# Kernel tuning notes

Measured on AMD Instinct MI355X. Metric: run time of the kernel, lower is better.

The kernel has to match this reference:

```python
import jax, jax.numpy as jnp
import numpy as np

B, TK, TL = 64, 2048, 256
V, E, KV, H, MH = 64, 256, 128, 512, 256
NLAYERS = 3
EPS = 1e-10


def _gumbel_softmax(rng, logits, temperature=1.0, eps=EPS):
    u = jax.random.uniform(rng, logits.shape, minval=0.0, maxval=1.0)
    noise = -jnp.log(-jnp.log(u + eps) + eps)
    return jax.nn.softmax((logits + noise) / temperature, axis=-1)


def setup_inputs() -> dict:
    key = jax.random.key(0)
    ks = jax.random.split(key, 32)
    s = 0.05
    inp = {
        "enc_key": jax.random.normal(ks[0], (B, TK, KV), jnp.float32),
        "value": jax.random.normal(ks[1], (B, TK, KV), jnp.float32),
        "labels_padded": jax.random.randint(ks[2], (TL, B), 0, V),
        "final_seq_lens": jax.random.randint(ks[3], (B,), 1, TK),
        "sos_token": 0,
        "teacher_forcing_ratio": 1,
        # embedding (Linear vocab->embed)
        "w_emb": jax.random.normal(ks[4], (E, V), jnp.float32) * s,
        "b_emb": jnp.zeros((E,), jnp.float32),
        # LSTMCell layer 0: input = embed + kv
        "w_ih0": jax.random.normal(ks[5], (4 * H, E + KV), jnp.float32) * s,
        "w_hh0": jax.random.normal(ks[6], (4 * H, H), jnp.float32) * s,
        "b_ih0": jnp.zeros((4 * H,), jnp.float32),
        "b_hh0": jnp.zeros((4 * H,), jnp.float32),
        # LSTMCell layers 1,2
        "w_ih1": jax.random.normal(ks[7], (4 * H, H), jnp.float32) * s,
        "w_hh1": jax.random.normal(ks[8], (4 * H, H), jnp.float32) * s,
        "b_ih1": jnp.zeros((4 * H,), jnp.float32),
        "b_hh1": jnp.zeros((4 * H,), jnp.float32),
        "w_ih2": jax.random.normal(ks[9], (4 * H, H), jnp.float32) * s,
        "w_hh2": jax.random.normal(ks[10], (4 * H, H), jnp.float32) * s,
        "b_ih2": jnp.zeros((4 * H,), jnp.float32),
        "b_hh2": jnp.zeros((4 * H,), jnp.float32),
        # fc: hidden -> key_value_size (query projection)
        "w_fc": jax.random.normal(ks[11], (KV, H), jnp.float32) * s,
        "b_fc": jnp.zeros((KV,), jnp.float32),
        # MLP: 2*kv -> mlp_hidden -> vocab, LeakyReLU(0.9)
        "w_mlp1": jax.random.normal(ks[12], (MH, 2 * KV), jnp.float32) * s,
        "b_mlp1": jnp.zeros((MH,), jnp.float32),
        "w_mlp2": jax.random.normal(ks[13], (V, MH), jnp.float32) * s,
        "b_mlp2": jnp.zeros((V,), jnp.float32),
    }
    return inp


def _lstm_cell(x, h, c, w_ih, w_hh, b_ih, b_hh):
    g = x @ w_ih.T + b_ih + h @ w_hh.T + b_hh
    i, f, gg, o = jnp.split(g, 4, axis=1)  # torch gate order i,f,g,o
    i, f, o = jax.nn.sigmoid(i), jax.nn.sigmoid(f), jax.nn.sigmoid(o)
    c2 = f * c + i * jnp.tanh(gg)
    h2 = o * jnp.tanh(c2)
    return h2, c2


def reference(enc_key, value, labels_padded, final_seq_lens, sos_token,
              teacher_forcing_ratio, w_emb, b_emb,
              w_ih0, w_hh0, b_ih0, b_hh0,
              w_ih1, w_hh1, b_ih1, b_hh1,
              w_ih2, w_hh2, b_ih2, b_hh2,
              w_fc, b_fc, w_mlp1, b_mlp1, w_mlp2, b_mlp2):
    # teacher_forcing_ratio == 1 -> always teacher forcing (faithful, deterministic)
    b, tk, kv = enc_key.shape
    tl = labels_padded.shape[0]
    v = w_emb.shape[1]
    rng = jax.random.key(42)
    k1, k2 = jax.random.split(rng)

    labels_onehot = jax.nn.one_hot(labels_padded, v, dtype=jnp.float32)  # [TL,B,V]
    labels_smoothed = _gumbel_softmax(k1, labels_onehot)
    sos_onehot = jax.nn.one_hot(jnp.full((b,), sos_token), v, dtype=jnp.float32)
    y0 = _gumbel_softmax(k2, sos_onehot)

    emb = lambda y: y @ w_emb.T + b_emb
    emb_labels = emb(labels_smoothed)           # [TL,B,E]
    emb_sos = emb(y0)                           # [B,E]
    # input embedding at step t is emb of teacher label t-1 (SOS at t=0)
    xs_emb = jnp.concatenate([emb_sos[None], emb_labels[:-1]], axis=0)

    mask = (jnp.arange(tk)[None, :] < final_seq_lens[:, None]).astype(enc_key.dtype)  # [B,TK]

    layer_params = [(w_ih0, w_hh0, b_ih0, b_hh0),
                    (w_ih1, w_hh1, b_ih1, b_hh1),
                    (w_ih2, w_hh2, b_ih2, b_hh2)]
    hdim = w_hh0.shape[1]
    z = jnp.zeros((b, hdim), enc_key.dtype)
    init = (tuple(z for _ in layer_params), tuple(z for _ in layer_params),
            jnp.zeros((b, kv), enc_key.dtype))

    def step(carry, emb_t):
        hs, cs, ctx = carry
        x = jnp.concatenate([emb_t, ctx], axis=1)
        new_h, new_c = [], []
        inp = x
        for (wi, wh, bi, bh), h, c in zip(layer_params, hs, cs):
            h2, c2 = _lstm_cell(inp, h, c, wi, wh, bi, bh)
            new_h.append(h2); new_c.append(c2)
            inp = h2
        query = new_h[-1] @ w_fc.T + b_fc                        # [B,KV]
        energy = jnp.einsum('btk,bk->bt', enc_key, query)        # [B,TK]
        attn = jax.nn.softmax(energy * mask, axis=1)             # mask-by-multiply, as original
        ctx2 = jnp.einsum('bt,btk->bk', attn, value)             # [B,KV]
        hid = jnp.concatenate([query, ctx2], axis=1)             # [B,2KV]
        h1 = hid @ w_mlp1.T + b_mlp1
        h1 = jnp.where(h1 >= 0, h1, 0.9 * h1)                    # LeakyReLU(0.9)
        y = h1 @ w_mlp2.T + b_mlp2                               # [B,V]
        return (tuple(new_h), tuple(new_c), ctx2), (y, attn)

    _, (y_hat, attns) = jax.lax.scan(step, init, xs_emb)
    y_hat = y_hat.transpose(1, 0, 2)                             # [B,TL,V]
    y_hat_label = jnp.argmax(y_hat, axis=2)                      # [B,TL]
    attentions = attns.transpose(1, 2, 0)                        # [B,TK,TL]
    return (y_hat, y_hat_label, labels_padded.T,
            labels_smoothed.transpose(1, 0, 2), attentions)
```

## Files before the change

kernel.cpp:

```cpp
#include <hip/hip_runtime.h>

typedef unsigned int u32;
typedef float nf4 __attribute__((ext_vector_type(4)));
#define DEVI __device__ __forceinline__

DEVI void tf2x32(u32 k0, u32 k1, u32 x0, u32 x1, u32& o0, u32& o1) {
  u32 ks2 = k0 ^ k1 ^ 0x1BD11BDAu;
  x0 += k0; x1 += k1;
#define TFR(r) { x0 += x1; x1 = (x1 << (r)) | (x1 >> (32 - (r))); x1 ^= x0; }
  TFR(13) TFR(15) TFR(26) TFR(6)
  x0 += k1; x1 += ks2 + 1u;
  TFR(17) TFR(29) TFR(16) TFR(24)
  x0 += ks2; x1 += k0 + 2u;
  TFR(13) TFR(15) TFR(26) TFR(6)
  x0 += k0; x1 += k1 + 3u;
  TFR(17) TFR(29) TFR(16) TFR(24)
  x0 += k1; x1 += ks2 + 4u;
  TFR(13) TFR(15) TFR(26) TFR(6)
  x0 += ks2; x1 += k0 + 5u;
#undef TFR
  o0 = x0; o1 = x1;
}

DEVI float jax_uniform(u32 k0, u32 k1, u32 idx) {
  u32 a, b; tf2x32(k0, k1, 0u, idx, a, b);
  u32 bits = a ^ b;
  return __uint_as_float((bits >> 9) | 0x3F800000u) - 1.0f;
}

DEVI float sigmoidf_(float x) { return 1.0f / (1.0f + expf(-x)); }

DEVI float AL(const float* p) {
  return __hip_atomic_load((float*)p, __ATOMIC_RELAXED, __HIP_MEMORY_SCOPE_AGENT);
}
DEVI void AS(float* p, float v) {
  __hip_atomic_store(p, v, __ATOMIC_RELAXED, __HIP_MEMORY_SCOPE_AGENT);
}

typedef const __attribute__((address_space(1))) u32* gas1;
typedef __attribute__((address_space(3))) u32* las3;
DEVI void gl16n(const float* g, float* l) { __builtin_amdgcn_global_load_lds((gas1)g, (las3)l, 16, 0, 0); }
#define WAITV(N) asm volatile("s_waitcnt vmcnt(" #N ")" ::: "memory")
#define SBAR __builtin_amdgcn_sched_barrier(0)

struct KArgs {
  const float* enc_key; const float* value;
  const int* labels; const int* seqlens; const int* sos;
  const float* w_emb; const float* b_emb;
  const float* w_ih0; const float* w_hh0; const float* b_ih0; const float* b_hh0;
  const float* w_ih1; const float* w_hh1; const float* b_ih1; const float* b_hh1;
  const float* w_ih2; const float* w_hh2; const float* b_ih2; const float* b_hh2;
  const float* w_fc; const float* b_fc;
  const float* w_mlp1; const float* b_mlp1;
  const float* w_mlp2; const float* b_mlp2;
  float* out; float* ws;
};

#define OF_Y0     0
#define OF_XEMB   4096
#define OF_HSB    4198400
#define OF_CSB    4395008
#define OF_CTX    4591616
#define OF_CTXQ   6696960
#define OF_MSQ    6729728
#define OF_QA     6730240
#define OF_WPK    8827392
#define OF_WFCT   14856704
#define OF_BC     14922240
#define OF_HT     14928384
#define OF_BAR    14993920
#define OF_QBAR   14998016
#define OF_ATT    14999040
#define WS_TOTAL  23387648
#define WP1 1835008
#define WP2 3932160

DEVI void bar_arrive_wait(int* bar, int& ep) {
  if (threadIdx.x == 0) {
    int g = (int)(blockIdx.x & 15);
    int old = __hip_atomic_fetch_add(bar + g * 64, 1, __ATOMIC_RELAXED, __HIP_MEMORY_SCOPE_AGENT);
    if (old == ep * 16 - 1) {
      int o2 = __hip_atomic_fetch_add(bar + 1024, 1, __ATOMIC_RELAXED, __HIP_MEMORY_SCOPE_AGENT);
      if (o2 == ep * 16 - 1) {
        #pragma unroll
        for (int gg = 0; gg < 16; ++gg)
          __hip_atomic_store(bar + 2048 + gg * 64, ep, __ATOMIC_RELAXED, __HIP_MEMORY_SCOPE_AGENT);
      }
    }
    while (__hip_atomic_load(bar + 2048 + g * 64, __ATOMIC_RELAXED, __HIP_MEMORY_SCOPE_AGENT) < ep)
      __builtin_amdgcn_s_sleep(1);
  }
  __syncthreads();
  ++ep;
}
DEVI void gridbar_fast(int* bar, int& ep) {
  WAITV(0);
  __syncthreads();
  bar_arrive_wait(bar, ep);
}
DEVI void gridbar_flush(int* bar, int& ep) {
  WAITV(0);
  __syncthreads();
  if (threadIdx.x == 0) __threadfence();
  __syncthreads();
  bar_arrive_wait(bar, ep);
  if (threadIdx.x == 0) __threadfence();
  __syncthreads();
}

__global__ void bar_init_kernel(int* bar) {
  for (int i = 0; i < 5; ++i) {
    int idx = threadIdx.x + i * 1024;
    if (idx < 5120) bar[idx] = 0;
  }
}

__global__ __launch_bounds__(1024, 1) void dec_kernel(KArgs A) {
  const int blk = blockIdx.x;
  const int tid = threadIdx.x;
  const int lane = tid & 63;
  const int w = tid >> 6;

  float* const Y0   = A.ws + OF_Y0;
  float* const XEMB = A.ws + OF_XEMB;
  float* const HSb  = A.ws + OF_HSB;
  float* const CSb  = A.ws + OF_CSB;
  float* const CTX  = A.ws + OF_CTX;
  float* const CTXQ = A.ws + OF_CTXQ;
  float* const MSQ  = A.ws + OF_MSQ;
  float* const QA   = A.ws + OF_QA;
  float* const WPACK= A.ws + OF_WPK;
  float* const WFCT = A.ws + OF_WFCT;
  float* const BC   = A.ws + OF_BC;
  float* const HT   = A.ws + OF_HT;
  int*   const bar  = (int*)(A.ws + OF_BAR);
  int*   const qbar = (int*)(A.ws + OF_QBAR);
  float* const ATTS = A.ws + OF_ATT + (size_t)blk * 32768;

  float* const out0 = A.out;
  float* const out1 = A.out + 1048576;
  float* const out2 = A.out + 1064960;
  float* const out3 = A.out + 1081344;
  float* const out4 = A.out + 2129920;

  __shared__ __align__(16) float SMf[39072];
  int ep = 1, eA = 1;

  const int rg = blk >> 2, bg = blk & 3;
  const int bq = rg, ch = bg;

  u32 KA0, KA1, KB0, KB1;
  tf2x32(0u, 42u, 0u, 0u, KA0, KA1);
  tf2x32(0u, 42u, 0u, 1u, KB0, KB1);

  if (bg == 0) {
    for (int idx = tid; idx < 28672; idx += 1024) {
      int tile = idx >> 12, rem = idx & 4095;
      int k = rem >> 5, slot = rem & 31;
      int pr = slot ^ ((k & 7) << 2);
      int g = pr >> 3, jj = pr & 7;
      int R = g * 512 + rg * 8 + jj;
      int gk = tile * 128 + k;
      WPACK[rg * 28672 + idx] = (gk < 384) ? A.w_ih0[R * 384 + gk] : A.w_hh0[R * 512 + gk - 384];
    }
    for (int idx = tid; idx < 32768; idx += 1024) {
      int tile = idx >> 12, rem = idx & 4095;
      int k = rem >> 5, slot = rem & 31;
      int pr = slot ^ ((k & 7) << 2);
      int g = pr >> 3, jj = pr & 7;
      int R = g * 512 + rg * 8 + jj;
      int gk = tile * 128 + k;
      WPACK[WP1 + rg * 32768 + idx] = (gk < 512) ? A.w_ih1[R * 512 + gk] : A.w_hh1[R * 512 + gk - 512];
    }
    for (int idx = tid; idx < 32768; idx += 1024) {
      int tile = idx >> 12, rem = idx & 4095;
      int k = rem >> 5, slot = rem & 31;
      int pr = slot ^ ((k & 7) << 2);
      int g = pr >> 3, jj = pr & 7;
      int R = g * 512 + rg * 8 + jj;
      int gk = tile * 128 + k;
      WPACK[WP2 + rg * 32768 + idx] = (gk < 512) ? A.w_ih2[R * 512 + gk] : A.w_hh2[R * 512 + gk - 512];
    }
  }
  if (blk < 65) {
    int slot = blk * 1024 + tid;
    int r = slot >> 2, q = slot & 3;
    if (r < 16448) {
      bool isY0 = (r >= 16384);
      int t = 0, b, label;
      u32 key0, key1, base;
      if (!isY0) {
        t = r >> 6; b = r & 63;
        label = A.labels[t * 64 + b];
        key0 = KA0; key1 = KA1; base = (u32)(r * 64);
      } else {
        b = r - 16384;
        label = A.sos[0];
        key0 = KB0; key1 = KB1; base = (u32)(b * 64);
      }
      float sv[16];
      float mx = -3.0e38f;
      #pragma unroll
      for (int j = 0; j < 16; ++j) {
        int v = (q << 4) + j;
        float u = jax_uniform(key0, key1, base + (u32)v);
        float inner = -logf(u + 1e-10f) + 1e-10f;
        float noise = -logf(inner);
        float s = noise + ((v == label) ? 1.0f : 0.0f);
        sv[j] = s; mx = fmaxf(mx, s);
      }
      mx = fmaxf(mx, __shfl_xor(mx, 1));
      mx = fmaxf(mx, __shfl_xor(mx, 2));
      float sum = 0.f;
      #pragma unroll
      for (int j = 0; j < 16; ++j) { sv[j] = expf(sv[j] - mx); sum += sv[j]; }
      sum += __shfl_xor(sum, 1);
      sum += __shfl_xor(sum, 2);
      float inv = 1.0f / sum;
      if (!isY0) {
        #pragma unroll
        for (int j = 0; j < 16; ++j) {
          int v = (q << 4) + j;
          out3[b * 16384 + t * 64 + v] = sv[j] * inv;
        }
        if (q == 0) out2[b * 256 + t] = (float)label;
      } else {
        #pragma unroll
        for (int j = 0; j < 16; ++j) Y0[b * 64 + (q << 4) + j] = sv[j] * inv;
      }
    }
  } else if (blk < 128) {
    const int total1 = 401408, total2 = 401408 + 65536;
    for (int idx = (blk - 65) * 1024 + tid; idx < total2; idx += 63 * 1024) {
      if (idx < total1) HSb[idx] = 0.f;
      else {
        int i2 = idx - total1;
        int kv = i2 >> 9, j = i2 & 511;
        WFCT[j * 128 + kv] = A.w_fc[kv * 512 + j];
      }
    }
  } else if (blk == 255) {
    for (int idx = tid; idx < 6144; idx += 1024) {
      int l = idx >> 11, r = idx & 2047;
      const float* bi = (l == 0) ? A.b_ih0 : (l == 1) ? A.b_ih1 : A.b_ih2;
      const float* bh = (l == 0) ? A.b_hh0 : (l == 1) ? A.b_hh1 : A.b_hh2;
      BC[idx] = bi[r] + bh[r];
    }
  }
  gridbar_flush(bar, ep);

  {
    const int t = blk;
    #pragma unroll
    for (int i = 0; i < 4; ++i) {
      int idx = tid + i * 1024;
      int b = idx >> 6, v = idx & 63;
      float sval = (t == 0) ? Y0[idx] : out3[b * 16384 + (t - 1) * 64 + v];
      SMf[b * 65 + v] = sval;
    }
    __syncthreads();
    const int b = lane;
    float* dst = XEMB + t * 16384;
    #pragma unroll 1
    for (int e0 = 0; e0 < 16; ++e0) {
      int e = w * 16 + e0;
      const float* we = A.w_emb + e * 64;
      float acc = A.b_emb[e];
      #pragma unroll 8
      for (int v = 0; v < 64; ++v) acc = fmaf(we[v], SMf[b * 65 + v], acc);
      dst[e * 64 + b] = acc;
    }
  }
  gridbar_flush(bar, ep);

  const int lenb = A.seqlens[bq];

#define KSTAGE(TILE, BUFI) { \
  const float* kgp_ = A.enc_key + (size_t)bq * 262144 + (size_t)(ch * 512 + (TILE) * 128) * 128; \
  float* dst_ = SMf + (BUFI) * 16384; \
  _Pragma("unroll") for (int s_ = 0; s_ < 4; ++s_) { \
    int i2_ = w * 4 + s_; int rr_ = 2 * i2_ + (lane >> 5); \
    gl16n(kgp_ + rr_ * 128 + (((lane & 31) ^ (rr_ & 7)) << 2), dst_ + i2_ * 256); } }
#define VSTAGE(TILE, BUFI) { \
  const float* vgp_ = A.value + (size_t)bq * 262144 + (size_t)(ch * 512 + (TILE) * 128) * 128; \
  float* dst_ = SMf + (BUFI) * 16384; \
  _Pragma("unroll") for (int s_ = 0; s_ < 4; ++s_) { \
    int i2_ = w * 4 + s_; \
    gl16n(vgp_ + i2_ * 256 + lane * 4, dst_ + i2_ * 256); } }

  #pragma unroll 1
  for (int t = 0; t < 256; ++t) {
    const int p = t & 1;

    #pragma unroll 1
    for (int l = 0; l < 3; ++l) {
      const int NT = (l == 0) ? 7 : 8;
      float* XL  = SMf;
      float* WL0 = SMf + 17408;
      float* WL1 = SMf + 21504;
      float* RED = SMf + 25600;

      const float* wpk = (l == 0) ? (WPACK + rg * 28672)
                       : (l == 1) ? (WPACK + WP1 + rg * 32768)
                                  : (WPACK + WP2 + rg * 32768);
      gl16n(wpk + w * 256 + lane * 4, WL0 + w * 256);

      if (l == 0) {
        const float* xe = XEMB + t * 16384;
        const float* ct = CTX + t * 8192;
        const float* h0 = HSb + p * 32768;
        #pragma unroll 2
        for (int m = 0; m < 14; ++m) {
          int idx = tid + m * 1024;
          int k = idx >> 4, bl = idx & 15;
          int bgl = bg * 16 + bl;
          float v;
          if (k < 256)      v = xe[k * 64 + bgl];
          else if (k < 384) v = AL(ct + (k - 256) * 64 + bgl);
          else              v = AL(h0 + (k - 384) * 64 + bgl);
          XL[k * 17 + bl] = v;
        }
      } else {
        const float* hin = HSb + ((l - 1) * 2 + (p ^ 1)) * 32768;
        const float* hpr = HSb + (l * 2 + p) * 32768;
        #pragma unroll 2
        for (int m = 0; m < 16; ++m) {
          int idx = tid + m * 1024;
          int k = idx >> 4, bl = idx & 15;
          int bgl = bg * 16 + bl;
          float v = (k < 512) ? AL(hin + k * 64 + bgl) : AL(hpr + (k - 512) * 64 + bgl);
          XL[k * 17 + bl] = v;
        }
      }

      const int g = w >> 2, kshi = w & 3;
      const int kslo = lane >> 3, bp = lane & 7;
      const int ks = kshi * 8 + kslo;
      float acc[16];
      #pragma unroll
      for (int i = 0; i < 16; ++i) acc[i] = 0.f;

      WAITV(0);
      __syncthreads();

      #pragma unroll 1
      for (int tile = 0; tile < NT; ++tile) {
        float* WLc = (tile & 1) ? WL1 : WL0;
        if (tile + 1 < NT) {
          float* WLn = ((tile + 1) & 1) ? WL1 : WL0;
          gl16n(wpk + (tile + 1) * 4096 + w * 256 + lane * 4, WLn + w * 256);
          WAITV(1);
        } else {
          WAITV(0);
        }
        __syncthreads();
        #pragma unroll
        for (int i = 0; i < 4; ++i) {
          int k = ks + 32 * i;
          int sw = (k & 7) << 2;
          const float* wb = WLc + k * 32;
          float4 wa = *(const float4*)&wb[(g * 8) ^ sw];
          float4 wv = *(const float4*)&wb[(g * 8 + 4) ^ sw];
          float x0 = XL[(tile * 128 + k) * 17 + bp * 2];
          float x1 = XL[(tile * 128 + k) * 17 + bp * 2 + 1];
          acc[0]  = fmaf(wa.x, x0, acc[0]);  acc[1]  = fmaf(wa.x, x1, acc[1]);
          acc[2]  = fmaf(wa.y, x0, acc[2]);  acc[3]  = fmaf(wa.y, x1, acc[3]);
          acc[4]  = fmaf(wa.z, x0, acc[4]);  acc[5]  = fmaf(wa.z, x1, acc[5]);
          acc[6]  = fmaf(wa.w, x0, acc[6]);  acc[7]  = fmaf(wa.w, x1, acc[7]);
          acc[8]  = fmaf(wv.x, x0, acc[8]);  acc[9]  = fmaf(wv.x, x1, acc[9]);
          acc[10] = fmaf(wv.y, x0, acc[10]); acc[11] = fmaf(wv.y, x1, acc[11]);
          acc[12] = fmaf(wv.z, x0, acc[12]); acc[13] = fmaf(wv.z, x1, acc[13]);
          acc[14] = fmaf(wv.w, x0, acc[14]); acc[15] = fmaf(wv.w, x1, acc[15]);
        }
        __syncthreads();
      }
      #pragma unroll
      for (int d = 8; d <= 32; d <<= 1) {
        #pragma unroll
        for (int i = 0; i < 16; ++i) acc[i] += __shfl_xor(acc[i], d);
      }
      if (kslo == 0) {
        #pragma unroll
        for (int i = 0; i < 16; ++i)
          RED[(g * 4 + kshi) * 128 + bp * 16 + i] = acc[i];
      }
      __syncthreads();
      if (tid < 128) {
        int jl = tid >> 4, bl = tid & 15;
        int j = rg * 8 + jl;
        int bgl = bg * 16 + bl;
        int ri = (bl >> 1) * 16 + jl * 2 + (bl & 1);
        float v0 = 0.f, v1 = 0.f, v2 = 0.f, v3 = 0.f;
        #pragma unroll
        for (int kh = 0; kh < 4; ++kh) {
          v0 += RED[(0 * 4 + kh) * 128 + ri];
          v1 += RED[(1 * 4 + kh) * 128 + ri];
          v2 += RED[(2 * 4 + kh) * 128 + ri];
          v3 += RED[(3 * 4 + kh) * 128 + ri];
        }
        float gi = v0 + BC[l * 2048 + j];
        float gf = v1 + BC[l * 2048 + 512 + j];
        float gG = v2 + BC[l * 2048 + 1024 + j];
        float go = v3 + BC[l * 2048 + 1536 + j];
        float cprev = AL(CSb + (l * 2 + p) * 32768 + j * 64 + bgl);
        float c2 = sigmoidf_(gf) * cprev + sigmoidf_(gi) * tanhf(gG);
        float h2 = sigmoidf_(go) * tanhf(c2);
        AS(CSb + (l * 2 + (p ^ 1)) * 32768 + j * 64 + bgl, c2);
        AS(HSb + (l * 2 + (p ^ 1)) * 32768 + j * 64 + bgl, h2);
        if (l == 2) AS(HT + (p ^ 1) * 32768 + bgl * 512 + j, h2);
      }
      gridbar_fast(bar, ep);
    }

    {
      float* H2C = SMf + 32768;
      float* QP  = SMf + 33280;
      float* QV  = SMf + 34304;
      float* ZS  = SMf + 34432;
      float* MR  = SMf + 34944;
      float* PR  = SMf + 34976;

      KSTAGE(0, 0); KSTAGE(1, 1);
      float h2v = 0.f;
      if (tid < 512) h2v = AL(HT + (p ^ 1) * 32768 + bq * 512 + tid);
      WAITV(0); SBAR;
      if (tid < 512) H2C[tid] = h2v;
      __syncthreads();
      {
        int kv = tid & 127, jg = tid >> 7;
        const float* wf = WFCT + (jg * 64) * 128 + kv;
        float pa = 0.f;
        #pragma unroll 8
        for (int jl = 0; jl < 64; ++jl) pa = fmaf(wf[jl * 128], H2C[jg * 64 + jl], pa);
        QP[jg * 128 + kv] = pa;
      }
      __syncthreads();
      if (tid < 128) {
        float qv = A.b_fc[tid];
        #pragma unroll
        for (int g = 0; g < 8; ++g) qv += QP[g * 128 + tid];
        QV[tid] = qv;
        if (ch == 0) QA[t * 8192 + tid * 64 + bq] = qv;
      }
      __syncthreads();

      #pragma unroll 1
      for (int tu = 0; tu < 4; ++tu) {
        {
          int tl = tid & 127, kq = tid >> 7, rot = tl & 7;
          const float* KB = SMf + (tu & 1) * 16384 + tl * 128;
          float e = 0.f;
          #pragma unroll
          for (int gi = 0; gi < 4; ++gi) {
            int g = kq * 4 + gi, slot = g ^ rot;
            float4 k4 = *(const float4*)&KB[slot * 4];
            float4 q4 = *(const float4*)&QV[g * 4];
            e += k4.x * q4.x + k4.y * q4.y + k4.z * q4.z + k4.w * q4.w;
          }
          QP[kq * 128 + tl] = e;
        }
        __syncthreads();
        if (tu == 0)      { KSTAGE(2, 0); }
        else if (tu == 1) { KSTAGE(3, 1); }
        else if (tu == 2) { VSTAGE(0, 0); }
        else              { VSTAGE(1, 1); }
        if (tid < 128) {
          float ee = 0.f;
          #pragma unroll
          for (int g = 0; g < 8; ++g) ee += QP[g * 128 + tid];
          int ta = ch * 512 + tu * 128 + tid;
          ZS[tu * 128 + tid] = (ta < lenb) ? ee : 0.0f;
        }
        if (tu < 3) { WAITV(4); }
        __syncthreads();
      }
      float z = (tid < 512) ? ZS[tid] : -3.0e38f;
      float mm = z;
      #pragma unroll
      for (int d = 1; d < 64; d <<= 1) mm = fmaxf(mm, __shfl_xor(mm, d));
      if (lane == 0 && w < 8) MR[w] = mm;
      __syncthreads();
      mm = MR[0];
      #pragma unroll
      for (int i2 = 1; i2 < 8; ++i2) mm = fmaxf(mm, MR[i2]);
      float ex = 0.f;
      if (tid < 512) { ex = expf(z - mm); ZS[tid] = ex; }
      float ss = ex;
      #pragma unroll
      for (int d = 1; d < 64; d <<= 1) ss += __shfl_xor(ss, d);
      if (lane == 0 && w < 8) MR[8 + w] = ss;
      __syncthreads();
      float S = 0.f;
      #pragma unroll
      for (int i2 = 0; i2 < 8; ++i2) S += MR[8 + i2];
      const float m_ch = mm;
      if (tid == 0) {
        AS(MSQ + bq * 8 + ch * 2, m_ch);
        AS(MSQ + bq * 8 + ch * 2 + 1, S);
      }
      float c0 = 0.f, c1 = 0.f, c2a = 0.f, c3 = 0.f;
      const int tg = tid >> 5, kv4 = (tid & 31) * 4;
      #pragma unroll 1
      for (int vt = 0; vt < 4; ++vt) {
        if (vt < 3) { WAITV(4); } else { WAITV(0); }
        __syncthreads();
        const float* B = SMf + (vt & 1) * 16384;
        #pragma unroll
        for (int i2 = 0; i2 < 4; ++i2) {
          int r = tg * 4 + i2;
          float a = ZS[vt * 128 + r];
          float4 v4 = *(const float4*)&B[r * 128 + kv4];
          c0 = fmaf(a, v4.x, c0); c1 = fmaf(a, v4.y, c1);
          c2a = fmaf(a, v4.z, c2a); c3 = fmaf(a, v4.w, c3);
        }
        __syncthreads();
        if (vt == 0)      { VSTAGE(2, 0); }
        else if (vt == 1) { VSTAGE(3, 1); }
      }
      PR[tg * 128 + kv4]     = c0;
      PR[tg * 128 + kv4 + 1] = c1;
      PR[tg * 128 + kv4 + 2] = c2a;
      PR[tg * 128 + kv4 + 3] = c3;
      __syncthreads();
      float ownpart = 0.f;
      if (tid < 128) {
        float s = 0.f;
        #pragma unroll
        for (int g2 = 0; g2 < 32; ++g2) s += PR[g2 * 128 + tid];
        ownpart = s;
        AS(CTXQ + bq * 512 + ch * 128 + tid, s);
      }
      WAITV(0);
      __syncthreads();
      if (tid == 0) {
        int* qc = qbar + bq * 8;
        __hip_atomic_fetch_add(qc, 1, __ATOMIC_RELAXED, __HIP_MEMORY_SCOPE_AGENT);
        while (__hip_atomic_load(qc, __ATOMIC_RELAXED, __HIP_MEMORY_SCOPE_AGENT) < eA * 4)
          __builtin_amdgcn_s_sleep(1);
      }
      __syncthreads();
      ++eA;
      if (tid < 8) MR[16 + tid] = AL(MSQ + bq * 8 + tid);
      __syncthreads();
      float mall = fmaxf(fmaxf(MR[16], MR[18]), fmaxf(MR[20], MR[22]));
      float Z = MR[17] * expf(MR[16] - mall) + MR[19] * expf(MR[18] - mall)
              + MR[21] * expf(MR[20] - mall) + MR[23] * expf(MR[22] - mall);
      float invZ = 1.0f / Z;
      if (tid < 512)
        ATTS[(size_t)(t & 63) * 512 + tid] = ZS[tid] * (expf(m_ch - mall) * invZ);
      if (ch == 0 && tid < 128) {
        float q1 = AL(CTXQ + bq * 512 + 128 + tid);
        float q2 = AL(CTXQ + bq * 512 + 256 + tid);
        float q3 = AL(CTXQ + bq * 512 + 384 + tid);
        float f0 = expf(MR[16] - mall) * invZ;
        float f1 = expf(MR[18] - mall) * invZ;
        float f2 = expf(MR[20] - mall) * invZ;
        float f3 = expf(MR[22] - mall) * invZ;
        AS(CTX + (t + 1) * 8192 + tid * 64 + bq,
           ownpart * f0 + q1 * f1 + q2 * f2 + q3 * f3);
      }
      if ((t & 63) == 63) {
        __syncthreads();
        if (tid < 512) {
          float* o4 = out4 + (size_t)bq * 524288 + (size_t)(ch * 512 + tid) * 256 + (t - 63);
          const float* sst = ATTS + tid;
          #pragma unroll 4
          for (int q4i = 0; q4i < 16; ++q4i) {
            nf4 v;
            v.x = sst[(size_t)(q4i * 4 + 0) * 512];
            v.y = sst[(size_t)(q4i * 4 + 1) * 512];
            v.z = sst[(size_t)(q4i * 4 + 2) * 512];
            v.w = sst[(size_t)(q4i * 4 + 3) * 512];
            __builtin_nontemporal_store(v, (nf4*)(o4 + q4i * 4));
          }
        }
      }
    }
    gridbar_fast(bar, ep);
  }

  gridbar_flush(bar, ep);

  {
    const int t = blk;
    const int sl = w, b = lane;
    const float* qa_t = QA + t * 8192;
    const float* ct1 = CTX + (t + 1) * 8192;
    #pragma unroll
    for (int i = 0; i < 8; ++i) {
      int idx = tid + i * 1024;
      SMf[(idx >> 6) * 65 + (idx & 63)] = qa_t[idx];
      SMf[(128 + (idx >> 6)) * 65 + (idx & 63)] = ct1[idx];
    }
    __syncthreads();
    float a1[16];
    #pragma unroll
    for (int i = 0; i < 16; ++i) a1[i] = 0.f;
    const float* w1 = A.w_mlp1 + (sl * 16) * 256;
    #pragma unroll 2
    for (int k = 0; k < 256; ++k) {
      float xv = SMf[k * 65 + b];
      #pragma unroll
      for (int m2 = 0; m2 < 16; ++m2) a1[m2] = fmaf(w1[m2 * 256 + k], xv, a1[m2]);
    }
    float* ACT = SMf + 16640;
    #pragma unroll
    for (int m2 = 0; m2 < 16; ++m2) {
      float v2 = a1[m2] + A.b_mlp1[sl * 16 + m2];
      ACT[(sl * 16 + m2) * 65 + b] = (v2 >= 0.f) ? v2 : 0.9f * v2;
    }
    __syncthreads();
    float y[4] = {0.f, 0.f, 0.f, 0.f};
    const float* w2 = A.w_mlp2 + (sl * 4) * 256;
    #pragma unroll 2
    for (int k = 0; k < 256; ++k) {
      float xv = ACT[k * 65 + b];
      #pragma unroll
      for (int m2 = 0; m2 < 4; ++m2) y[m2] = fmaf(w2[m2 * 256 + k], xv, y[m2]);
    }
    #pragma unroll
    for (int m2 = 0; m2 < 4; ++m2) y[m2] += A.b_mlp2[sl * 4 + m2];
    *(float4*)(out0 + b * 16384 + t * 64 + sl * 4) = make_float4(y[0], y[1], y[2], y[3]);
    __syncthreads();
    float* YB = SMf + 34976;
    #pragma unroll
    for (int m2 = 0; m2 < 4; ++m2) YB[(sl * 4 + m2) * 65 + b] = y[m2];
    __syncthreads();
    if (tid < 64) {
      float best = YB[tid];
      int bi = 0;
      #pragma unroll 1
      for (int v = 1; v < 64; ++v) {
        float val = YB[v * 65 + tid];
        if (val > best) { best = val; bi = v; }
      }
      out1[tid * 256 + t] = (float)bi;
    }
  }
}

// ... 31 lines not shown
```

Before: 28.76 ms.

## Deepen weight prefetch pipeline and overlap activation gathers and key staging

Activation gathers for each LSTM layer are now loaded into registers first, then the first two weight tiles are issued before the register values are stored to shared memory. The tile loop prefetches two tiles ahead instead of one, issuing each prefetch after the compute barrier. The attention key staging (KSTAGE) for the next phase now starts before the layer-2 grid barrier so its loads overlap the barrier wait. This targets latency exposed on the serial recurrent path, at the cost of more registers and extra block barriers.

```diff
diff --git a/kernel.cpp b/kernel.cpp
--- a/kernel.cpp
+++ b/kernel.cpp
@@ -303,35 +303,50 @@
       const float* wpk = (l == 0) ? (WPACK + rg * 28672)
                        : (l == 1) ? (WPACK + WP1 + rg * 32768)
                                   : (WPACK + WP2 + rg * 32768);
-      gl16n(wpk + w * 256 + lane * 4, WL0 + w * 256);
-
+
+      float xr[16];
       if (l == 0) {
         const float* xe = XEMB + t * 16384;
         const float* ct = CTX + t * 8192;
         const float* h0 = HSb + p * 32768;
-        #pragma unroll 2
+        #pragma unroll
         for (int m = 0; m < 14; ++m) {
           int idx = tid + m * 1024;
           int k = idx >> 4, bl = idx & 15;
           int bgl = bg * 16 + bl;
-          float v;
-          if (k < 256)      v = xe[k * 64 + bgl];
-          else if (k < 384) v = AL(ct + (k - 256) * 64 + bgl);
-          else              v = AL(h0 + (k - 384) * 64 + bgl);
-          XL[k * 17 + bl] = v;
+          xr[m] = (k < 256) ? xe[k * 64 + bgl]
+                : (k < 384) ? AL(ct + (k - 256) * 64 + bgl)
+                            : AL(h0 + (k - 384) * 64 + bgl);
         }
       } else {
         const float* hin = HSb + ((l - 1) * 2 + (p ^ 1)) * 32768;
         const float* hpr = HSb + (l * 2 + p) * 32768;
-        #pragma unroll 2
+        #pragma unroll
         for (int m = 0; m < 16; ++m) {
           int idx = tid + m * 1024;
           int k = idx >> 4, bl = idx & 15;
           int bgl = bg * 16 + bl;
-          float v = (k < 512) ? AL(hin + k * 64 + bgl) : AL(hpr + (k - 512) * 64 + bgl);
-          XL[k * 17 + bl] = v;
-        }
-      }
+          xr[m] = (k < 512) ? AL(hin + k * 64 + bgl) : AL(hpr + (k - 512) * 64 + bgl);
+        }
+      }
+      SBAR;
+      gl16n(wpk + w * 256 + lane * 4, WL0 + w * 256);
+      gl16n(wpk + 4096 + w * 256 + lane * 4, WL1 + w * 256);
+      WAITV(2); SBAR;
+      if (l == 0) {
+        #pragma unroll
+        for (int m = 0; m < 14; ++m) {
+          int idx = tid + m * 1024;
+          XL[(idx >> 4) * 17 + (idx & 15)] = xr[m];
+        }
+      } else {
+        #pragma unroll
+        for (int m = 0; m < 16; ++m) {
+          int idx = tid + m * 1024;
+          XL[(idx >> 4) * 17 + (idx & 15)] = xr[m];
+        }
+      }
+      __syncthreads();
 
       const int g = w >> 2, kshi = w & 3;
       const int kslo = lane >> 3, bp = lane & 7;
@@ -340,19 +355,10 @@
       #pragma unroll
       for (int i = 0; i < 16; ++i) acc[i] = 0.f;
 
-      WAITV(0);
-      __syncthreads();
-
       #pragma unroll 1
       for (int tile = 0; tile < NT; ++tile) {
         float* WLc = (tile & 1) ? WL1 : WL0;
-        if (tile + 1 < NT) {
-          float* WLn = ((tile + 1) & 1) ? WL1 : WL0;
-          gl16n(wpk + (tile + 1) * 4096 + w * 256 + lane * 4, WLn + w * 256);
-          WAITV(1);
-        } else {
-          WAITV(0);
-        }
+        if (tile + 1 < NT) { WAITV(1); } else { WAITV(0); }
         __syncthreads();
         #pragma unroll
         for (int i = 0; i < 4; ++i) {
@@ -373,6 +379,10 @@
           acc[14] = fmaf(wv.w, x0, acc[14]); acc[15] = fmaf(wv.w, x1, acc[15]);
         }
         __syncthreads();
+        if (tile + 2 < NT) {
+          float* WLn = (tile & 1) ? WL1 : WL0;
+          gl16n(wpk + (tile + 2) * 4096 + w * 256 + lane * 4, WLn + w * 256);
+        }
       }
       #pragma unroll
       for (int d = 8; d <= 32; d <<= 1) {
@@ -409,6 +419,11 @@
         AS(HSb + (l * 2 + (p ^ 1)) * 32768 + j * 64 + bgl, h2);
         if (l == 2) AS(HT + (p ^ 1) * 32768 + bgl * 512 + j, h2);
       }
+      if (l == 2) {
+        __syncthreads();
+        KSTAGE(0, 0);
+        KSTAGE(1, 1);
+      }
       gridbar_fast(bar, ep);
     }
 
@@ -420,7 +435,6 @@
       float* MR  = SMf + 34944;
       float* PR  = SMf + 34976;
 
-      KSTAGE(0, 0); KSTAGE(1, 1);
       float h2v = 0.f;
       if (tid < 512) h2v = AL(HT + (p ^ 1) * 32768 + bq * 512 + tid);
       WAITV(0); SBAR;
```

After: 28.20 ms. About the same (-1.9%).

## Keep LSTM weight slices resident in LDS and split K across blocks

Applied to the files above, without the earlier changes.

Each block now loads its slice of the three LSTM layers' weights (8 rows x 4 gates, a quarter of K) into shared memory once, instead of streaming packed weight tiles from global memory every timestep. The gate reduction is split along K across the 4 blocks of a row group. Partial sums go to a global PART buffer and are combined by one block after a per-group counter wait. The fc query projection is split across the 4 chunk blocks with a group barrier. Key and value staging moves to 64-row tiles issued early, before the layer-2 grid barrier. This trades repeated weight traffic for extra partial-sum writes, more group barriers, and a smaller attention staging buffer.

```diff
diff --git a/kernel.cpp b/kernel.cpp
--- a/kernel.cpp
+++ b/kernel.cpp
@@ -64,16 +64,15 @@
 #define OF_CTXQ   6696960
 #define OF_MSQ    6729728
 #define OF_QA     6730240
-#define OF_WPK    8827392
-#define OF_WFCT   14856704
+#define OF_QWS    8827392
+#define OF_PART   8835584
 #define OF_BC     14922240
 #define OF_HT     14928384
 #define OF_BAR    14993920
 #define OF_QBAR   14998016
 #define OF_ATT    14999040
 #define WS_TOTAL  23387648
-#define WP1 1835008
-#define WP2 3932160
+
 
 DEVI void bar_arrive_wait(int* bar, int& ep) {
   if (threadIdx.x == 0) {
@@ -129,8 +128,8 @@
   float* const CTXQ = A.ws + OF_CTXQ;
   float* const MSQ  = A.ws + OF_MSQ;
   float* const QA   = A.ws + OF_QA;
-  float* const WPACK= A.ws + OF_WPK;
-  float* const WFCT = A.ws + OF_WFCT;
+  float* const QWS  = A.ws + OF_QWS;
+  float* const PART = A.ws + OF_PART;
   float* const BC   = A.ws + OF_BC;
   float* const HT   = A.ws + OF_HT;
   int*   const bar  = (int*)(A.ws + OF_BAR);
@@ -143,45 +142,16 @@
   float* const out3 = A.out + 1081344;
   float* const out4 = A.out + 2129920;
 
-  __shared__ __align__(16) float SMf[39072];
-  int ep = 1, eA = 1;
-
-  const int rg = blk >> 2, bg = blk & 3;
-  const int bq = rg, ch = bg;
+  __shared__ __align__(16) float SMf[40960];
+  int ep = 1, eL = 1, eA = 1;
+
+  const int rg = blk >> 2, kg = blk & 3;
+  const int bq = rg, ch = kg;
 
   u32 KA0, KA1, KB0, KB1;
   tf2x32(0u, 42u, 0u, 0u, KA0, KA1);
   tf2x32(0u, 42u, 0u, 1u, KB0, KB1);
 
-  if (bg == 0) {
-    for (int idx = tid; idx < 28672; idx += 1024) {
-      int tile = idx >> 12, rem = idx & 4095;
-      int k = rem >> 5, slot = rem & 31;
-      int pr = slot ^ ((k & 7) << 2);
-      int g = pr >> 3, jj = pr & 7;
-      int R = g * 512 + rg * 8 + jj;
-      int gk = tile * 128 + k;
-      WPACK[rg * 28672 + idx] = (gk < 384) ? A.w_ih0[R * 384 + gk] : A.w_hh0[R * 512 + gk - 384];
-    }
-    for (int idx = tid; idx < 32768; idx += 1024) {
-      int tile = idx >> 12, rem = idx & 4095;
-      int k = rem >> 5, slot = rem & 31;
-      int pr = slot ^ ((k & 7) << 2);
-      int g = pr >> 3, jj = pr & 7;
-      int R = g * 512 + rg * 8 + jj;
-      int gk = tile * 128 + k;
-      WPACK[WP1 + rg * 32768 + idx] = (gk < 512) ? A.w_ih1[R * 512 + gk] : A.w_hh1[R * 512 + gk - 512];
-    }
-    for (int idx = tid; idx < 32768; idx += 1024) {
-      int tile = idx >> 12, rem = idx & 4095;
-      int k = rem >> 5, slot = rem & 31;
-      int pr = slot ^ ((k & 7) << 2);
-      int g = pr >> 3, jj = pr & 7;
-      int R = g * 512 + rg * 8 + jj;
-      int gk = tile * 128 + k;
-      WPACK[WP2 + rg * 32768 + idx] = (gk < 512) ? A.w_ih2[R * 512 + gk] : A.w_hh2[R * 512 + gk - 512];
-    }
-  }
   if (blk < 65) {
     int slot = blk * 1024 + tid;
     int r = slot >> 2, q = slot & 3;
@@ -230,15 +200,8 @@
       }
     }
   } else if (blk < 128) {
-    const int total1 = 401408, total2 = 401408 + 65536;
-    for (int idx = (blk - 65) * 1024 + tid; idx < total2; idx += 63 * 1024) {
-      if (idx < total1) HSb[idx] = 0.f;
-      else {
-        int i2 = idx - total1;
-        int kv = i2 >> 9, j = i2 & 511;
-        WFCT[j * 128 + kv] = A.w_fc[kv * 512 + j];
-      }
-    }
+    for (int idx = (blk - 65) * 1024 + tid; idx < 401408; idx += 63 * 1024)
+      HSb[idx] = 0.f;
   } else if (blk == 255) {
     for (int idx = tid; idx < 6144; idx += 1024) {
       int l = idx >> 11, r = idx & 2047;
@@ -273,20 +236,59 @@
   }
   gridbar_flush(bar, ep);
 
+  {
+    __syncthreads();
+    #pragma unroll 1
+    for (int it = 0; it < 8; ++it) {
+      int idx = tid + it * 1024;
+      int ri = idx >> 8, kk = idx & 255;
+      if (kk < 224) {
+        int R = (ri >> 3) * 512 + rg * 8 + (ri & 7);
+        int gk = kg * 224 + kk;
+        SMf[ri * 224 + kk] = (gk < 384) ? A.w_ih0[R * 384 + gk] : A.w_hh0[R * 512 + gk - 384];
+      }
+    }
+    #pragma unroll 1
+    for (int it = 0; it < 8; ++it) {
+      int idx = tid + it * 1024;
+      int ri = idx >> 8, kk = idx & 255;
+      int R = (ri >> 3) * 512 + rg * 8 + (ri & 7);
+      int gk = kg * 256 + kk;
+      SMf[7168 + ri * 256 + kk] = (gk < 512) ? A.w_ih1[R * 512 + gk] : A.w_hh1[R * 512 + gk - 512];
+    }
+    #pragma unroll 1
+    for (int it = 0; it < 8; ++it) {
+      int idx = tid + it * 1024;
+      int ri = idx >> 8, kk = idx & 255;
+      int R = (ri >> 3) * 512 + rg * 8 + (ri & 7);
+      int gk = kg * 256 + kk;
+      SMf[15360 + ri * 256 + kk] = (gk < 512) ? A.w_ih2[R * 512 + gk] : A.w_hh2[R * 512 + gk - 512];
+    }
+    __syncthreads();
+  }
+
   const int lenb = A.seqlens[bq];
-
-#define KSTAGE(TILE, BUFI) { \
-  const float* kgp_ = A.enc_key + (size_t)bq * 262144 + (size_t)(ch * 512 + (TILE) * 128) * 128; \
-  float* dst_ = SMf + (BUFI) * 16384; \
-  _Pragma("unroll") for (int s_ = 0; s_ < 4; ++s_) { \
-    int i2_ = w * 4 + s_; int rr_ = 2 * i2_ + (lane >> 5); \
-    gl16n(kgp_ + rr_ * 128 + (((lane & 31) ^ (rr_ & 7)) << 2), dst_ + i2_ * 256); } }
-#define VSTAGE(TILE, BUFI) { \
-  const float* vgp_ = A.value + (size_t)bq * 262144 + (size_t)(ch * 512 + (TILE) * 128) * 128; \
-  float* dst_ = SMf + (BUFI) * 16384; \
-  _Pragma("unroll") for (int s_ = 0; s_ < 4; ++s_) { \
-    int i2_ = w * 4 + s_; \
-    gl16n(vgp_ + i2_ * 256 + lane * 4, dst_ + i2_ * 256); } }
+  float* const XL   = SMf + 23552;
+  float* const KTB0 = SMf + 23552;
+  float* const KTB1 = SMf + 31744;
+  float* const H2C  = SMf + 39936;
+  float* const QVb  = SMf + 39936;
+  float* const MRb  = SMf + 40064;
+  float* const ZSb  = SMf + 40448;
+  float* const PRb  = SMf + 23552;
+
+#define KST64(TILE, BUFI) { \
+  const float* kp_ = A.enc_key + (size_t)bq * 262144 + (size_t)(ch * 512 + (TILE) * 64) * 128; \
+  float* d_ = SMf + 23552 + (BUFI) * 8192; \
+  _Pragma("unroll") for (int s_ = 0; s_ < 2; ++s_) { \
+    int i_ = w * 2 + s_; \
+    gl16n(kp_ + (2 * i_ + (lane >> 5)) * 128 + (lane & 31) * 4, d_ + i_ * 256); } }
+#define VST64(TILE, BUFI) { \
+  const float* vp_ = A.value + (size_t)bq * 262144 + (size_t)(ch * 512 + (TILE) * 64) * 128; \
+  float* d_ = SMf + 23552 + (BUFI) * 8192; \
+  _Pragma("unroll") for (int s_ = 0; s_ < 2; ++s_) { \
+    int i_ = w * 2 + s_; \
+    gl16n(vp_ + (2 * i_ + (lane >> 5)) * 128 + (lane & 31) * 4, d_ + i_ * 256); } }
 
   #pragma unroll 1
   for (int t = 0; t < 256; ++t) {
@@ -294,268 +296,243 @@
 
     #pragma unroll 1
     for (int l = 0; l < 3; ++l) {
-      const int NT = (l == 0) ? 7 : 8;
-      float* XL  = SMf;
-      float* WL0 = SMf + 17408;
-      float* WL1 = SMf + 21504;
-      float* RED = SMf + 25600;
-
-      const float* wpk = (l == 0) ? (WPACK + rg * 28672)
-                       : (l == 1) ? (WPACK + WP1 + rg * 32768)
-                                  : (WPACK + WP2 + rg * 32768);
-      gl16n(wpk + w * 256 + lane * 4, WL0 + w * 256);
-
+      const int Kq  = (l == 0) ? 224 : 256;
+      const int NXR = (l == 0) ? 14 : 16;
+      const int WOFF = (l == 0) ? 0 : (l == 1) ? 7168 : 15360;
+
+      float xr[16];
       if (l == 0) {
         const float* xe = XEMB + t * 16384;
         const float* ct = CTX + t * 8192;
         const float* h0 = HSb + p * 32768;
-        #pragma unroll 2
+        #pragma unroll
         for (int m = 0; m < 14; ++m) {
           int idx = tid + m * 1024;
-          int k = idx >> 4, bl = idx & 15;
-          int bgl = bg * 16 + bl;
-          float v;
-          if (k < 256)      v = xe[k * 64 + bgl];
-          else if (k < 384) v = AL(ct + (k - 256) * 64 + bgl);
-          else              v = AL(h0 + (k - 384) * 64 + bgl);
-          XL[k * 17 + bl] = v;
+          int k = idx >> 6, b = idx & 63;
+          int gk = kg * 224 + k;
+          xr[m] = (gk < 256) ? xe[gk * 64 + b]
+                : (gk < 384) ? AL(ct + (gk - 256) * 64 + b)
+                             : AL(h0 + (gk - 384) * 64 + b);
         }
       } else {
         const float* hin = HSb + ((l - 1) * 2 + (p ^ 1)) * 32768;
         const float* hpr = HSb + (l * 2 + p) * 32768;
-        #pragma unroll 2
+        #pragma unroll
         for (int m = 0; m < 16; ++m) {
           int idx = tid + m * 1024;
-          int k = idx >> 4, bl = idx & 15;
-          int bgl = bg * 16 + bl;
-          float v = (k < 512) ? AL(hin + k * 64 + bgl) : AL(hpr + (k - 512) * 64 + bgl);
-          XL[k * 17 + bl] = v;
-        }
-      }
-
-      const int g = w >> 2, kshi = w & 3;
-      const int kslo = lane >> 3, bp = lane & 7;
-      const int ks = kshi * 8 + kslo;
-      float acc[16];
-      #pragma unroll
-      for (int i = 0; i < 16; ++i) acc[i] = 0.f;
-
+          int k = idx >> 6, b = idx & 63;
+          int gk = kg * 256 + k;
+          xr[m] = (gk < 512) ? AL(hin + gk * 64 + b) : AL(hpr + (gk - 512) * 64 + b);
+        }
+      }
+      SBAR; WAITV(0); SBAR;
+      #pragma unroll
+      for (int m = 0; m < 16; ++m) {
+        if (m < NXR) {
+          int idx = tid + m * 1024;
+          XL[(idx >> 6) * 64 + (idx & 63)] = xr[m];
+        }
+      }
+      __syncthreads();
+
+      float a0 = 0.f, a1 = 0.f;
+      {
+        const float* wr0 = SMf + WOFF + (2 * w) * Kq;
+        const float* wr1 = SMf + WOFF + (2 * w + 1) * Kq;
+        const float* xb = XL + lane;
+        #pragma unroll 4
+        for (int k4 = 0; k4 < Kq / 4; ++k4) {
+          float4 w0 = *(const float4*)(wr0 + k4 * 4);
+          float4 w1 = *(const float4*)(wr1 + k4 * 4);
+          float x0 = xb[(k4 * 4 + 0) * 64];
+          float x1 = xb[(k4 * 4 + 1) * 64];
+          float x2 = xb[(k4 * 4 + 2) * 64];
+          float x3 = xb[(k4 * 4 + 3) * 64];
+          a0 = fmaf(w0.w, x3, fmaf(w0.z, x2, fmaf(w0.y, x1, fmaf(w0.x, x0, a0))));
+          a1 = fmaf(w1.w, x3, fmaf(w1.z, x2, fmaf(w1.y, x1, fmaf(w1.x, x0, a1))));
+        }
+      }
+      {
+        float* pb = PART + blk * 2048;
+        AS(pb + (2 * w) * 64 + lane, a0);
+        AS(pb + (2 * w + 1) * 64 + lane, a1);
+      }
       WAITV(0);
       __syncthreads();
-
-      #pragma unroll 1
-      for (int tile = 0; tile < NT; ++tile) {
-        float* WLc = (tile & 1) ? WL1 : WL0;
-        if (tile + 1 < NT) {
-          float* WLn = ((tile + 1) & 1) ? WL1 : WL0;
-          gl16n(wpk + (tile + 1) * 4096 + w * 256 + lane * 4, WLn + w * 256);
-          WAITV(1);
-        } else {
-          WAITV(0);
-        }
-        __syncthreads();
-        #pragma unroll
-        for (int i = 0; i < 4; ++i) {
-          int k = ks + 32 * i;
-          int sw = (k & 7) << 2;
-          const float* wb = WLc + k * 32;
-          float4 wa = *(const float4*)&wb[(g * 8) ^ sw];
-          float4 wv = *(const float4*)&wb[(g * 8 + 4) ^ sw];
-          float x0 = XL[(tile * 128 + k) * 17 + bp * 2];
-          float x1 = XL[(tile * 128 + k) * 17 + bp * 2 + 1];
-          acc[0]  = fmaf(wa.x, x0, acc[0]);  acc[1]  = fmaf(wa.x, x1, acc[1]);
-          acc[2]  = fmaf(wa.y, x0, acc[2]);  acc[3]  = fmaf(wa.y, x1, acc[3]);
-          acc[4]  = fmaf(wa.z, x0, acc[4]);  acc[5]  = fmaf(wa.z, x1, acc[5]);
-          acc[6]  = fmaf(wa.w, x0, acc[6]);  acc[7]  = fmaf(wa.w, x1, acc[7]);
-          acc[8]  = fmaf(wv.x, x0, acc[8]);  acc[9]  = fmaf(wv.x, x1, acc[9]);
-          acc[10] = fmaf(wv.y, x0, acc[10]); acc[11] = fmaf(wv.y, x1, acc[11]);
-          acc[12] = fmaf(wv.z, x0, acc[12]); acc[13] = fmaf(wv.z, x1, acc[13]);
-          acc[14] = fmaf(wv.w, x0, acc[14]); acc[15] = fmaf(wv.w, x1, acc[15]);
-        }
-        __syncthreads();
-      }
-      #pragma unroll
-      for (int d = 8; d <= 32; d <<= 1) {
-        #pragma unroll
-        for (int i = 0; i < 16; ++i) acc[i] += __shfl_xor(acc[i], d);
-      }
-      if (kslo == 0) {
-        #pragma unroll
-        for (int i = 0; i < 16; ++i)
-          RED[(g * 4 + kshi) * 128 + bp * 16 + i] = acc[i];
-      }
-      __syncthreads();
-      if (tid < 128) {
-        int jl = tid >> 4, bl = tid & 15;
+      if (tid == 0) {
+        int* qc = qbar + rg * 8;
+        __hip_atomic_fetch_add(qc, 1, __ATOMIC_RELAXED, __HIP_MEMORY_SCOPE_AGENT);
+        if (kg == 0)
+          while (__hip_atomic_load(qc, __ATOMIC_RELAXED, __HIP_MEMORY_SCOPE_AGENT) < eL * 4)
+            __builtin_amdgcn_s_sleep(1);
+      }
+      __syncthreads();
+      ++eL;
+      if (kg == 0 && tid < 512) {
+        int jl = tid >> 6, b = tid & 63;
         int j = rg * 8 + jl;
-        int bgl = bg * 16 + bl;
-        int ri = (bl >> 1) * 16 + jl * 2 + (bl & 1);
-        float v0 = 0.f, v1 = 0.f, v2 = 0.f, v3 = 0.f;
-        #pragma unroll
-        for (int kh = 0; kh < 4; ++kh) {
-          v0 += RED[(0 * 4 + kh) * 128 + ri];
-          v1 += RED[(1 * 4 + kh) * 128 + ri];
-          v2 += RED[(2 * 4 + kh) * 128 + ri];
-          v3 += RED[(3 * 4 + kh) * 128 + ri];
-        }
-        float gi = v0 + BC[l * 2048 + j];
-        float gf = v1 + BC[l * 2048 + 512 + j];
-        float gG = v2 + BC[l * 2048 + 1024 + j];
-        float go = v3 + BC[l * 2048 + 1536 + j];
-        float cprev = AL(CSb + (l * 2 + p) * 32768 + j * 64 + bgl);
+        const float* base = PART + rg * 4 * 2048;
+        float pr[16];
+        #pragma unroll
+        for (int g = 0; g < 4; ++g)
+          #pragma unroll
+          for (int q = 0; q < 4; ++q)
+            pr[g * 4 + q] = AL(base + q * 2048 + (g * 8 + jl) * 64 + b);
+        float cprev = AL(CSb + (l * 2 + p) * 32768 + j * 64 + b);
+        SBAR;
+        float gi = pr[0] + pr[1] + pr[2] + pr[3]     + BC[l * 2048 + j];
+        float gf = pr[4] + pr[5] + pr[6] + pr[7]     + BC[l * 2048 + 512 + j];
+        float gG = pr[8] + pr[9] + pr[10] + pr[11]   + BC[l * 2048 + 1024 + j];
+        float go = pr[12] + pr[13] + pr[14] + pr[15] + BC[l * 2048 + 1536 + j];
         float c2 = sigmoidf_(gf) * cprev + sigmoidf_(gi) * tanhf(gG);
         float h2 = sigmoidf_(go) * tanhf(c2);
-        AS(CSb + (l * 2 + (p ^ 1)) * 32768 + j * 64 + bgl, c2);
-        AS(HSb + (l * 2 + (p ^ 1)) * 32768 + j * 64 + bgl, h2);
-        if (l == 2) AS(HT + (p ^ 1) * 32768 + bgl * 512 + j, h2);
-      }
-      gridbar_fast(bar, ep);
+        AS(CSb + (l * 2 + (p ^ 1)) * 32768 + j * 64 + b, c2);
+        AS(HSb + (l * 2 + (p ^ 1)) * 32768 + j * 64 + b, h2);
+        if (l == 2) AS(HT + (p ^ 1) * 32768 + b * 512 + j, h2);
+      }
+      if (l < 2) {
+        gridbar_fast(bar, ep);
+      } else {
+        WAITV(0);
+        __syncthreads();
+        KST64(0, 0);
+        KST64(1, 1);
+        bar_arrive_wait(bar, ep);
+      }
     }
 
     {
-      float* H2C = SMf + 32768;
-      float* QP  = SMf + 33280;
-      float* QV  = SMf + 34304;
-      float* ZS  = SMf + 34432;
-      float* MR  = SMf + 34944;
-      float* PR  = SMf + 34976;
-
-      KSTAGE(0, 0); KSTAGE(1, 1);
       float h2v = 0.f;
       if (tid < 512) h2v = AL(HT + (p ^ 1) * 32768 + bq * 512 + tid);
-      WAITV(0); SBAR;
+      SBAR; WAITV(0); SBAR;
       if (tid < 512) H2C[tid] = h2v;
       __syncthreads();
       {
-        int kv = tid & 127, jg = tid >> 7;
-        const float* wf = WFCT + (jg * 64) * 128 + kv;
+        int kvq = ch * 32 + (tid >> 5), jseg = tid & 31;
+        const float* wf = A.w_fc + kvq * 512 + jseg * 16;
         float pa = 0.f;
-        #pragma unroll 8
-        for (int jl = 0; jl < 64; ++jl) pa = fmaf(wf[jl * 128], H2C[jg * 64 + jl], pa);
-        QP[jg * 128 + kv] = pa;
-      }
-      __syncthreads();
-      if (tid < 128) {
-        float qv = A.b_fc[tid];
-        #pragma unroll
-        for (int g = 0; g < 8; ++g) qv += QP[g * 128 + tid];
-        QV[tid] = qv;
-        if (ch == 0) QA[t * 8192 + tid * 64 + bq] = qv;
-      }
-      __syncthreads();
-
+        #pragma unroll
+        for (int i = 0; i < 16; ++i) pa = fmaf(wf[i], H2C[jseg * 16 + i], pa);
+        #pragma unroll
+        for (int d = 1; d < 32; d <<= 1) pa += __shfl_xor(pa, d);
+        if (jseg == 0) AS(QWS + bq * 128 + kvq, pa + A.b_fc[kvq]);
+      }
+      WAITV(0);
+      __syncthreads();
+      if (tid == 0) {
+        int* qc = qbar + 512 + bq * 8;
+        __hip_atomic_fetch_add(qc, 1, __ATOMIC_RELAXED, __HIP_MEMORY_SCOPE_AGENT);
+        while (__hip_atomic_load(qc, __ATOMIC_RELAXED, __HIP_MEMORY_SCOPE_AGENT) < eA * 4)
+          __builtin_amdgcn_s_sleep(1);
+      }
+      __syncthreads();
+      ++eA;
+      {
+        float qv = 0.f;
+        if (tid < 128) qv = AL(QWS + bq * 128 + tid);
+        SBAR; WAITV(0); SBAR;
+        if (tid < 128) {
+          QVb[tid] = qv;
+          if (ch == 0) QA[t * 8192 + tid * 64 + bq] = qv;
+        }
+      }
+      __syncthreads();
+      const int tl = tid >> 4, seg = tid & 15;
+      float qr[8];
+      #pragma unroll
+      for (int i = 0; i < 8; ++i) qr[i] = QVb[seg + 16 * i];
       #pragma unroll 1
-      for (int tu = 0; tu < 4; ++tu) {
-        {
-          int tl = tid & 127, kq = tid >> 7, rot = tl & 7;
-          const float* KB = SMf + (tu & 1) * 16384 + tl * 128;
-          float e = 0.f;
-          #pragma unroll
-          for (int gi = 0; gi < 4; ++gi) {
-            int g = kq * 4 + gi, slot = g ^ rot;
-            float4 k4 = *(const float4*)&KB[slot * 4];
-            float4 q4 = *(const float4*)&QV[g * 4];
-            e += k4.x * q4.x + k4.y * q4.y + k4.z * q4.z + k4.w * q4.w;
-          }
-          QP[kq * 128 + tl] = e;
-        }
+      for (int tu = 0; tu < 8; ++tu) {
+        if (tu >= 2) { if (tu == 7) { WAITV(0); } else { WAITV(2); } }
         __syncthreads();
-        if (tu == 0)      { KSTAGE(2, 0); }
-        else if (tu == 1) { KSTAGE(3, 1); }
-        else if (tu == 2) { VSTAGE(0, 0); }
-        else              { VSTAGE(1, 1); }
-        if (tid < 128) {
-          float ee = 0.f;
-          #pragma unroll
-          for (int g = 0; g < 8; ++g) ee += QP[g * 128 + tid];
-          int ta = ch * 512 + tu * 128 + tid;
-          ZS[tu * 128 + tid] = (ta < lenb) ? ee : 0.0f;
-        }
-        if (tu < 3) { WAITV(4); }
+        const float* KB = (tu & 1) ? KTB1 : KTB0;
+        float e = 0.f;
+        #pragma unroll
+        for (int i = 0; i < 8; ++i) e = fmaf(KB[tl * 128 + seg + 16 * i], qr[i], e);
+        #pragma unroll
+        for (int d = 1; d < 16; d <<= 1) e += __shfl_xor(e, d);
+        int ta = ch * 512 + tu * 64 + tl;
+        if (seg == 0) ZSb[tu * 64 + tl] = (ta < lenb) ? e : 0.0f;
         __syncthreads();
-      }
-      float z = (tid < 512) ? ZS[tid] : -3.0e38f;
+        if (tu + 2 < 8) { KST64(tu + 2, (tu & 1)); }
+      }
+      VST64(0, 0);
+      VST64(1, 1);
+      float z = (tid < 512) ? ZSb[tid] : -3.0e38f;
       float mm = z;
       #pragma unroll
       for (int d = 1; d < 64; d <<= 1) mm = fmaxf(mm, __shfl_xor(mm, d));
-      if (lane == 0 && w < 8) MR[w] = mm;
-      __syncthreads();
-      mm = MR[0];
-      #pragma unroll
-      for (int i2 = 1; i2 < 8; ++i2) mm = fmaxf(mm, MR[i2]);
+      if (lane == 0 && w < 8) MRb[w] = mm;
+      __syncthreads();
+      mm = MRb[0];
+      #pragma unroll
+      for (int i2 = 1; i2 < 8; ++i2) mm = fmaxf(mm, MRb[i2]);
       float ex = 0.f;
-      if (tid < 512) { ex = expf(z - mm); ZS[tid] = ex; }
+      if (tid < 512) { ex = expf(z - mm); ZSb[tid] = ex; }
       float ss = ex;
       #pragma unroll
       for (int d = 1; d < 64; d <<= 1) ss += __shfl_xor(ss, d);
-      if (lane == 0 && w < 8) MR[8 + w] = ss;
+      if (lane == 0 && w < 8) MRb[8 + w] = ss;
       __syncthreads();
       float S = 0.f;
       #pragma unroll
-      for (int i2 = 0; i2 < 8; ++i2) S += MR[8 + i2];
+      for (int i2 = 0; i2 < 8; ++i2) S += MRb[8 + i2];
       const float m_ch = mm;
       if (tid == 0) {
         AS(MSQ + bq * 8 + ch * 2, m_ch);
         AS(MSQ + bq * 8 + ch * 2 + 1, S);
       }
-      float c0 = 0.f, c1 = 0.f, c2a = 0.f, c3 = 0.f;
-      const int tg = tid >> 5, kv4 = (tid & 31) * 4;
+      const int kv = tid & 127, tg = tid >> 7;
+      float cacc = 0.f;
       #pragma unroll 1
-      for (int vt = 0; vt < 4; ++vt) {
-        if (vt < 3) { WAITV(4); } else { WAITV(0); }
+      for (int vt = 0; vt < 8; ++vt) {
+        if (vt == 7) { WAITV(0); } else { WAITV(2); }
         __syncthreads();
-        const float* B = SMf + (vt & 1) * 16384;
-        #pragma unroll
-        for (int i2 = 0; i2 < 4; ++i2) {
-          int r = tg * 4 + i2;
-          float a = ZS[vt * 128 + r];
-          float4 v4 = *(const float4*)&B[r * 128 + kv4];
-          c0 = fmaf(a, v4.x, c0); c1 = fmaf(a, v4.y, c1);
-          c2a = fmaf(a, v4.z, c2a); c3 = fmaf(a, v4.w, c3);
+        const float* VB = (vt & 1) ? KTB1 : KTB0;
+        #pragma unroll
+        for (int i = 0; i < 8; ++i) {
+          int r = tg * 8 + i;
+          cacc = fmaf(ZSb[vt * 64 + r], VB[r * 128 + kv], cacc);
         }
         __syncthreads();
-        if (vt == 0)      { VSTAGE(2, 0); }
-        else if (vt == 1) { VSTAGE(3, 1); }
-      }
-      PR[tg * 128 + kv4]     = c0;
-      PR[tg * 128 + kv4 + 1] = c1;
-      PR[tg * 128 + kv4 + 2] = c2a;
-      PR[tg * 128 + kv4 + 3] = c3;
+        if (vt + 2 < 8) { VST64(vt + 2, (vt & 1)); }
+      }
+      PRb[tg * 128 + kv] = cacc;
       __syncthreads();
       float ownpart = 0.f;
       if (tid < 128) {
         float s = 0.f;
         #pragma unroll
-        for (int g2 = 0; g2 < 32; ++g2) s += PR[g2 * 128 + tid];
+        for (int g2 = 0; g2 < 8; ++g2) s += PRb[g2 * 128 + tid];
         ownpart = s;
         AS(CTXQ + bq * 512 + ch * 128 + tid, s);
       }
       WAITV(0);
       __syncthreads();
       if (tid == 0) {
-        int* qc = qbar + bq * 8;
+        int* qc = qbar + 512 + bq * 8;
         __hip_atomic_fetch_add(qc, 1, __ATOMIC_RELAXED, __HIP_MEMORY_SCOPE_AGENT);
         while (__hip_atomic_load(qc, __ATOMIC_RELAXED, __HIP_MEMORY_SCOPE_AGENT) < eA * 4)
           __builtin_amdgcn_s_sleep(1);
       }
       __syncthreads();
       ++eA;
-      if (tid < 8) MR[16 + tid] = AL(MSQ + bq * 8 + tid);
-      __syncthreads();
-      float mall = fmaxf(fmaxf(MR[16], MR[18]), fmaxf(MR[20], MR[22]));
-      float Z = MR[17] * expf(MR[16] - mall) + MR[19] * expf(MR[18] - mall)
-              + MR[21] * expf(MR[20] - mall) + MR[23] * expf(MR[22] - mall);
+      if (tid < 8) MRb[16 + tid] = AL(MSQ + bq * 8 + tid);
+      __syncthreads();
+      float mall = fmaxf(fmaxf(MRb[16], MRb[18]), fmaxf(MRb[20], MRb[22]));
+      float Z = MRb[17] * expf(MRb[16] - mall) + MRb[19] * expf(MRb[18] - mall)
+              + MRb[21] * expf(MRb[20] - mall) + MRb[23] * expf(MRb[22] - mall);
       float invZ = 1.0f / Z;
       if (tid < 512)
-        ATTS[(size_t)(t & 63) * 512 + tid] = ZS[tid] * (expf(m_ch - mall) * invZ);
+        ATTS[(size_t)(t & 63) * 512 + tid] = ZSb[tid] * (expf(m_ch - mall) * invZ);
       if (ch == 0 && tid < 128) {
         float q1 = AL(CTXQ + bq * 512 + 128 + tid);
         float q2 = AL(CTXQ + bq * 512 + 256 + tid);
         float q3 = AL(CTXQ + bq * 512 + 384 + tid);
-        float f0 = expf(MR[16] - mall) * invZ;
-        float f1 = expf(MR[18] - mall) * invZ;
-        float f2 = expf(MR[20] - mall) * invZ;
-        float f3 = expf(MR[22] - mall) * invZ;
+        float f0 = expf(MRb[16] - mall) * invZ;
+        float f1 = expf(MRb[18] - mall) * invZ;
+        float f2 = expf(MRb[20] - mall) * invZ;
+        float f3 = expf(MRb[22] - mall) * invZ;
         AS(CTX + (t + 1) * 8192 + tid * 64 + bq,
            ownpart * f0 + q1 * f1 + q2 * f2 + q3 * f3);
       }
```

Result: slower. 37.23 ms (+29.4%).
